# Optimization experiments

Hardware: AMD Instinct MI355X
Metric: run time of the kernel (lower is better)

Reference implementation:

```python
import jax, jax.numpy as jnp
import numpy as np

WS = 7          # window size
HEADS = 8
SHIFT = WS // 2  # shift=True -> 3
C = 256
KD = C // HEADS  # key_dim = 32
LN_EPS = 1e-3    # keras LayerNormalization default


def setup_inputs() -> dict:
    key = jax.random.key(0)
    ks = jax.random.split(key, 12)
    s = 1.0 / np.sqrt(C)
    x = jax.random.normal(ks[0], (16, 112, 112, C), dtype=jnp.float32)
    wq = jax.random.normal(ks[1], (C, HEADS, KD), dtype=jnp.float32) * s
    bq = jnp.zeros((HEADS, KD), dtype=jnp.float32)
    wk = jax.random.normal(ks[2], (C, HEADS, KD), dtype=jnp.float32) * s
    bk = jnp.zeros((HEADS, KD), dtype=jnp.float32)
    wv = jax.random.normal(ks[3], (C, HEADS, KD), dtype=jnp.float32) * s
    bv = jnp.zeros((HEADS, KD), dtype=jnp.float32)
    wo = jax.random.normal(ks[4], (HEADS, KD, C), dtype=jnp.float32) * s
    bo = jnp.zeros((C,), dtype=jnp.float32)
    gamma = jnp.ones((C,), dtype=jnp.float32)
    beta = jnp.zeros((C,), dtype=jnp.float32)
    return {"x": x, "wq": wq, "bq": bq, "wk": wk, "bk": bk,
            "wv": wv, "bv": bv, "wo": wo, "bo": bo,
            "gamma": gamma, "beta": beta}


def _swin_window_attn(x, wq, bq, wk, bk, wv, bv, wo, bo, gamma, beta):
    b, h, w, c = x.shape
    pad_h = (WS - h % WS) % WS
    pad_w = (WS - w % WS) % WS
    if pad_h or pad_w:
        x = jnp.pad(x, ((0, 0), (0, pad_h), (0, pad_w), (0, 0)))
    hp, wp = h + pad_h, w + pad_w
    if SHIFT > 0:
        x = jnp.roll(x, shift=(-SHIFT, -SHIFT), axis=(1, 2))
    nh, nw = hp // WS, wp // WS
    # window partition: (b, nh, WS, nw, WS, c) -> (b*nh*nw, WS*WS, c)
    win = x.reshape(b, nh, WS, nw, WS, c).transpose(0, 1, 3, 2, 4, 5)
    win = win.reshape(b * nh * nw, WS * WS, c)
    # multi-head attention (keras MHA: query scaled by 1/sqrt(key_dim))
    q = jnp.einsum("nsc,chd->nshd", win, wq) + bq
    k = jnp.einsum("nsc,chd->nshd", win, wk) + bk
    v = jnp.einsum("nsc,chd->nshd", win, wv) + bv
    scores = jnp.einsum("nqhd,nkhd->nhqk", q, k) / jnp.sqrt(jnp.float32(KD)).astype(q.dtype)
    probs = jax.nn.softmax(scores, axis=-1)
    ctx = jnp.einsum("nhqk,nkhd->nqhd", probs, v)
    attn = jnp.einsum("nqhd,hdc->nqc", ctx, wo) + bo
    # residual + LayerNorm
    y = attn + win
    mu = jnp.mean(y, axis=-1, keepdims=True)
    var = jnp.mean(jnp.square(y - mu), axis=-1, keepdims=True)
    y = (y - mu) * jax.lax.rsqrt(var + LN_EPS) * gamma + beta
    # window reverse
    out = y.reshape(b, nh, nw, WS, WS, c).transpose(0, 1, 3, 2, 4, 5)
    out = out.reshape(b, hp, wp, c)
    if SHIFT > 0:
        out = jnp.roll(out, shift=(SHIFT, SHIFT), axis=(1, 2))
    if pad_h or pad_w:
        out = out[:, :h, :w, :]
    return out


def reference(x, wq, bq, wk, bk, wv, bv, wo, bo, gamma, beta):
    return _swin_window_attn(x, wq, bq, wk, bk, wv, bv, wo, bo, gamma, beta)
```

## Files before the change

### kernel.cpp

```cpp
#include <hip/hip_runtime.h>
#include <hip/hip_bf16.h>

typedef __attribute__((ext_vector_type(8))) short short8;
typedef __attribute__((ext_vector_type(4))) short short4v;
typedef __attribute__((ext_vector_type(4))) float float4v;

#define LDS_BYTES 144384
#define XBF_OFF   0
#define VT_OFF    33792
#define Q_OFF     70656
#define K_OFF     104448
#define P_OFF     70656
#define CTX_OFF   33792
#define Y_OFF     70656

__device__ __forceinline__ unsigned short f2bf(float f) {
    union { float f; unsigned int u; } v; v.f = f;
    unsigned int r = v.u + 0x7FFFu + ((v.u >> 16) & 1u);
    return (unsigned short)(r >> 16);
}
__device__ __forceinline__ float bf2f(unsigned short h) {
    union { unsigned int u; float f; } v; v.u = ((unsigned int)h) << 16;
    return v.f;
}

__global__ void prep_weights(const float* __restrict__ wq, const float* __restrict__ wk,
                             const float* __restrict__ wv, const float* __restrict__ wo,
                             unsigned short* __restrict__ wfrag) {
    int tid = blockIdx.x * 256 + threadIdx.x;
    if (tid >= 4 * 65536) return;
    int m = tid >> 16;
    int e = tid & 65535;
    int j = e & 7;
    int lane = (e >> 3) & 63;
    int nt2 = (e >> 9) & 15;
    int ks = e >> 13;
    int c = ks * 32 + (lane >> 4) * 8 + j;
    int o = nt2 * 16 + (lane & 15);
    const float* W = (m == 0) ? wq : (m == 1) ? wk : (m == 2) ? wv : wo;
    wfrag[tid] = f2bf(W[c * 256 + o]);
}

__global__ __launch_bounds__(1024, 4) void swin_fused(
    const float* __restrict__ x,
    const unsigned short* __restrict__ wfrag,
    const float* __restrict__ bq, const float* __restrict__ bk,
    const float* __restrict__ bv, const float* __restrict__ bo,
    const float* __restrict__ gamma, const float* __restrict__ beta,
    float* __restrict__ out)
{
    extern __shared__ char smem[];
    const int tid = threadIdx.x;
    const int w    = tid >> 6;
    const int h    = w & 7;
    const int half = w >> 3;
    const int l   = tid & 63;
    const int l15 = l & 15;
    const int l4  = l >> 4;
    const int nt2 = 2 * h + half;

    const int blk = blockIdx.x;
    const int bb  = blk >> 8;
    const int wh  = (blk >> 4) & 15;
    const int ww  = blk & 15;

    unsigned short* Xbf = (unsigned short*)(smem + XBF_OFF);

    for (int idx = tid; idx < 64 * 64; idx += 1024) {
        const int tok = idx >> 6;
        const int c4  = idx & 63;
        float4v f = (float4v){0.f, 0.f, 0.f, 0.f};
        if (tok < 49) {
            const int i = tok / 7;
            const int j = tok - 7 * i;
            int gr = wh * 7 + i + 3; if (gr >= 112) gr -= 112;
            int gc = ww * 7 + j + 3; if (gc >= 112) gc -= 112;
            f = *(const float4v*)(x + (((size_t)bb * 112 + gr) * 112 + gc) * 256 + c4 * 4);
        }
        short4v hv;
        hv.x = (short)f2bf(f.x); hv.y = (short)f2bf(f.y);
        hv.z = (short)f2bf(f.z); hv.w = (short)f2bf(f.w);
        *(short4v*)(Xbf + tok * 264 + c4 * 4) = hv;
    }
    __syncthreads();

    unsigned short* Qs = (unsigned short*)(smem + Q_OFF);
    unsigned short* Ks = (unsigned short*)(smem + K_OFF);
    unsigned short* Vt = (unsigned short*)(smem + VT_OFF);

    const float* biases[3] = { bq, bk, bv };
#pragma unroll
    for (int m = 0; m < 3; ++m) {
        float4v acc[4];
#pragma unroll
        for (int mt = 0; mt < 4; ++mt) acc[mt] = (float4v){0.f, 0.f, 0.f, 0.f};
        const unsigned short* wmat = wfrag + m * 65536;
#pragma unroll
        for (int ks = 0; ks < 8; ++ks) {
            short8 bfr = *(const short8*)(wmat + ((ks * 16 + nt2) * 64 + l) * 8);
#pragma unroll
            for (int mt = 0; mt < 4; ++mt) {
                short8 afr = *(const short8*)(Xbf + (mt * 16 + l15) * 264 + ks * 32 + l4 * 8);
                acc[mt] = __builtin_amdgcn_mfma_f32_16x16x32_bf16(afr, bfr, acc[mt], 0, 0, 0);
            }
        }
        const int o = nt2 * 16 + l15;
        const float bias = biases[m][o];
        if (m == 2) {
            const int d = half * 16 + l15;
#pragma unroll
            for (int mt = 0; mt < 4; ++mt) {
                short4v hv;
                hv.x = (short)f2bf(acc[mt][0] + bias);
                hv.y = (short)f2bf(acc[mt][1] + bias);
                hv.z = (short)f2bf(acc[mt][2] + bias);
                hv.w = (short)f2bf(acc[mt][3] + bias);
                *(short4v*)(Vt + h * 2304 + d * 72 + mt * 16 + l4 * 4) = hv;
            }
        } else {
            unsigned short* dst = (m == 0) ? Qs : Ks;
#pragma unroll
            for (int mt = 0; mt < 4; ++mt) {
                const int tok0 = mt * 16 + l4 * 4;
                dst[(tok0 + 0) * 264 + o] = f2bf(acc[mt][0] + bias);
                dst[(tok0 + 1) * 264 + o] = f2bf(acc[mt][1] + bias);
                dst[(tok0 + 2) * 264 + o] = f2bf(acc[mt][2] + bias);
                dst[(tok0 + 3) * 264 + o] = f2bf(acc[mt][3] + bias);
            }
        }
    }
    __syncthreads();

    float4v sa[4][2];
#pragma unroll
    for (int mt = 0; mt < 4; ++mt)
#pragma unroll
        for (int nt = 0; nt < 2; ++nt)
            sa[mt][nt] = (float4v){0.f, 0.f, 0.f, 0.f};
    {
        short8 kfr[4], qfr[2];
#pragma unroll
        for (int mt = 0; mt < 4; ++mt)
            kfr[mt] = *(const short8*)(Ks + (mt * 16 + l15) * 264 + 32 * h + l4 * 8);
#pragma unroll
        for (int nt = 0; nt < 2; ++nt)
            qfr[nt] = *(const short8*)(Qs + (32 * half + nt * 16 + l15) * 264 + 32 * h + l4 * 8);
#pragma unroll
        for (int mt = 0; mt < 4; ++mt)
#pragma unroll
            for (int nt = 0; nt < 2; ++nt)
                sa[mt][nt] = __builtin_amdgcn_mfma_f32_16x16x32_bf16(kfr[mt], qfr[nt], sa[mt][nt], 0, 0, 0);
    }
    __syncthreads();

    unsigned short* Ph = (unsigned short*)(smem + P_OFF) + h * 4608;
    const float SCALE = 0.17677669529663687f;
#pragma unroll
    for (int nt = 0; nt < 2; ++nt) {
        float sv[4][4];
        float mx = -1e30f;
#pragma unroll
        for (int mt = 0; mt < 4; ++mt)
#pragma unroll
            for (int r = 0; r < 4; ++r) {
                const bool valid = (mt < 3) || ((l4 == 0) && (r == 0));
                sv[mt][r] = valid ? sa[mt][nt][r] * SCALE : -1e30f;
                mx = fmaxf(mx, sv[mt][r]);
            }
        mx = fmaxf(mx, __shfl_xor(mx, 16, 64));
        mx = fmaxf(mx, __shfl_xor(mx, 32, 64));
        float p[4][4];
        float sum = 0.f;
#pragma unroll
        for (int mt = 0; mt < 4; ++mt)
#pragma unroll
            for (int r = 0; r < 4; ++r) {
                p[mt][r] = __expf(sv[mt][r] - mx);
                sum += p[mt][r];
            }
        sum += __shfl_xor(sum, 16, 64);
        sum += __shfl_xor(sum, 32, 64);
        const float inv = 1.f / sum;
        const int q = 32 * half + nt * 16 + l15;
#pragma unroll
        for (int mt = 0; mt < 4; ++mt) {
            short4v hv;
            hv.x = (short)f2bf(p[mt][0] * inv);
            hv.y = (short)f2bf(p[mt][1] * inv);
            hv.z = (short)f2bf(p[mt][2] * inv);
            hv.w = (short)f2bf(p[mt][3] * inv);
            *(short4v*)(Ph + q * 72 + mt * 16 + l4 * 4) = hv;
        }
    }

    float4v ca[2][2];
#pragma unroll
    for (int mtl = 0; mtl < 2; ++mtl)
#pragma unroll
        for (int nt = 0; nt < 2; ++nt)
            ca[mtl][nt] = (float4v){0.f, 0.f, 0.f, 0.f};
#pragma unroll
    for (int ks = 0; ks < 2; ++ks) {
        short8 afr[2];
#pragma unroll
        for (int mtl = 0; mtl < 2; ++mtl)
            afr[mtl] = *(const short8*)(Ph + (32 * half + mtl * 16 + l15) * 72 + ks * 32 + l4 * 8);
#pragma unroll
        for (int nt = 0; nt < 2; ++nt) {
            short8 bfr = *(const short8*)(Vt + h * 2304 + (nt * 16 + l15) * 72 + ks * 32 + l4 * 8);
#pragma unroll
            for (int mtl = 0; mtl < 2; ++mtl)
                ca[mtl][nt] = __builtin_amdgcn_mfma_f32_16x16x32_bf16(afr[mtl], bfr, ca[mtl][nt], 0, 0, 0);
        }
    }
    __syncthreads();

    unsigned short* Ctx = (unsigned short*)(smem + CTX_OFF);
#pragma unroll
    for (int nt = 0; nt < 2; ++nt) {
        const int o = 32 * h + nt * 16 + l15;
#pragma unroll
        for (int mtl = 0; mtl < 2; ++mtl) {
            const int tok0 = (2 * half + mtl) * 16 + l4 * 4;
            Ctx[(tok0 + 0) * 264 + o] = f2bf(ca[mtl][nt][0]);
            Ctx[(tok0 + 1) * 264 + o] = f2bf(ca[mtl][nt][1]);
            Ctx[(tok0 + 2) * 264 + o] = f2bf(ca[mtl][nt][2]);
            Ctx[(tok0 + 3) * 264 + o] = f2bf(ca[mtl][nt][3]);
        }
    }
    __syncthreads();

    float4v oa[4];
#pragma unroll
    for (int mt = 0; mt < 4; ++mt) oa[mt] = (float4v){0.f, 0.f, 0.f, 0.f};
    const unsigned short* womat = wfrag + 3 * 65536;
#pragma unroll
    for (int ks = 0; ks < 8; ++ks) {
        short8 bfr = *(const short8*)(womat + ((ks * 16 + nt2) * 64 + l) * 8);
#pragma unroll
        for (int mt = 0; mt < 4; ++mt) {
            short8 afr = *(const short8*)(Ctx + (mt * 16 + l15) * 264 + ks * 32 + l4 * 8);
            oa[mt] = __builtin_amdgcn_mfma_f32_16x16x32_bf16(afr, bfr, oa[mt], 0, 0, 0);
        }
    }
    float* Y = (float*)(smem + Y_OFF);
    {
        const int cout = nt2 * 16 + l15;
        const float bias = bo[cout];
#pragma unroll
        for (int mt = 0; mt < 4; ++mt)
#pragma unroll
            for (int r = 0; r < 4; ++r) {
                const int tok = mt * 16 + l4 * 4 + r;
                const float xv = bf2f(Xbf[tok * 264 + cout]);
                Y[tok * 260 + cout] = oa[mt][r] + bias + xv;
            }
    }
    __syncthreads();

    const float4v g4  = *(const float4v*)(gamma + l * 4);
    const float4v be4 = *(const float4v*)(beta + l * 4);
#pragma unroll
    for (int t = 0; t < 4; ++t) {
        const int tok = w + t * 16;
        if (tok < 49) {
            float4v f = *(const float4v*)(Y + tok * 260 + l * 4);
            float sum = f.x + f.y + f.z + f.w;
            float sq  = f.x * f.x + f.y * f.y + f.z * f.z + f.w * f.w;
#pragma unroll
            for (int msk = 1; msk < 64; msk <<= 1) {
                sum += __shfl_xor(sum, msk, 64);
                sq  += __shfl_xor(sq,  msk, 64);
            }
            const float mu   = sum * (1.f / 256.f);
            const float var  = sq * (1.f / 256.f) - mu * mu;
            const float rstd = rsqrtf(var + 1e-3f);
            const int i = tok / 7;
            const int j = tok - 7 * i;
            int gr = wh * 7 + i + 3; if (gr >= 112) gr -= 112;
            int gc = ww * 7 + j + 3; if (gc >= 112) gc -= 112;
            float4v o4;
            o4.x = (f.x - mu) * rstd * g4.x + be4.x;
            o4.y = (f.y - mu) * rstd * g4.y + be4.y;
            o4.z = (f.z - mu) * rstd * g4.z + be4.z;
            o4.w = (f.w - mu) * rstd * g4.w + be4.w;
            *(float4v*)(out + (((size_t)bb * 112 + gr) * 112 + gc) * 256 + l * 4) = o4;
        }
    }
}

extern "C" void kernel_launch(void* const* d_in, const int* in_sizes, int n_in,
                              void* d_out, int out_size, void* d_ws, size_t ws_size,
                              hipStream_t stream) {
    const float* x     = (const float*)d_in[0];
    const float* wq    = (const float*)d_in[1];
    const float* bq    = (const float*)d_in[2];
    const float* wk    = (const float*)d_in[3];
    const float* bk    = (const float*)d_in[4];
    const float* wv    = (const float*)d_in[5];
    const float* bv    = (const float*)d_in[6];
    const float* wo    = (const float*)d_in[7];
    const float* bo    = (const float*)d_in[8];
    const float* gamma = (const float*)d_in[9];
    const float* beta  = (const float*)d_in[10];
    float* out = (float*)d_out;
    unsigned short* wfrag = (unsigned short*)d_ws;

    prep_weights<<<1024, 256, 0, stream>>>(wq, wk, wv, wo, wfrag);

    hipFuncSetAttribute((const void*)swin_fused,
                        hipFuncAttributeMaxDynamicSharedMemorySize, LDS_BYTES);
    swin_fused<<<4096, 1024, LDS_BYTES, stream>>>(x, wfrag, bq, bk, bv, bo, gamma, beta, out);
}
```

Measured before the change: 302.8 us.

## XOR-swizzle LDS row layout, use packed bf16 conversions, raise MFMA wave priority

```diff
diff --git a/kernel.cpp b/kernel.cpp
--- a/kernel.cpp
+++ b/kernel.cpp
@@ -4,6 +4,7 @@
 typedef __attribute__((ext_vector_type(8))) short short8;
 typedef __attribute__((ext_vector_type(4))) short short4v;
 typedef __attribute__((ext_vector_type(4))) float float4v;
+typedef __attribute__((ext_vector_type(2))) unsigned int uint2v;
 
 #define LDS_BYTES 144384
 #define XBF_OFF   0
@@ -14,10 +15,16 @@
 #define CTX_OFF   33792
 #define Y_OFF     70656
 
-__device__ __forceinline__ unsigned short f2bf(float f) {
-    union { float f; unsigned int u; } v; v.f = f;
-    unsigned int r = v.u + 0x7FFFu + ((v.u >> 16) & 1u);
-    return (unsigned short)(r >> 16);
+
+__device__ __forceinline__ unsigned short f2bf_rn(float f) {
+    union { __hip_bfloat16 b; unsigned short u; } v;
+    v.b = __float2bfloat16(f);
+    return v.u;
+}
+__device__ __forceinline__ unsigned int pk2bf(float a, float b) {
+    union { __hip_bfloat162 h; unsigned int u; } v;
+    v.h = __float22bfloat162_rn(make_float2(a, b));
+    return v.u;
 }
 __device__ __forceinline__ float bf2f(unsigned short h) {
     union { unsigned int u; float f; } v; v.u = ((unsigned int)h) << 16;
@@ -38,7 +45,7 @@
     int c = ks * 32 + (lane >> 4) * 8 + j;
     int o = nt2 * 16 + (lane & 15);
     const float* W = (m == 0) ? wq : (m == 1) ? wk : (m == 2) ? wv : wo;
-    wfrag[tid] = f2bf(W[c * 256 + o]);
+    wfrag[tid] = f2bf_rn(W[c * 256 + o]);
 }
 
 __global__ __launch_bounds__(1024, 4) void swin_fused(
@@ -59,12 +66,15 @@
     const int l4  = l >> 4;
     const int nt2 = 2 * h + half;
 
+    const int sxA = (l15 & 8) << 2;
+    const int sxS = (l4  & 2) << 4;
+
     const int blk = blockIdx.x;
     const int bb  = blk >> 8;
     const int wh  = (blk >> 4) & 15;
     const int ww  = blk & 15;
 
-    unsigned short* Xbf = (unsigned short*)(smem + XBF_OFF);
+    char* XbfC = smem + XBF_OFF;
 
     for (int idx = tid; idx < 64 * 64; idx += 1024) {
         const int tok = idx >> 6;
@@ -77,15 +87,15 @@
             int gc = ww * 7 + j + 3; if (gc >= 112) gc -= 112;
             f = *(const float4v*)(x + (((size_t)bb * 112 + gr) * 112 + gc) * 256 + c4 * 4);
         }
-        short4v hv;
-        hv.x = (short)f2bf(f.x); hv.y = (short)f2bf(f.y);
-        hv.z = (short)f2bf(f.z); hv.w = (short)f2bf(f.w);
-        *(short4v*)(Xbf + tok * 264 + c4 * 4) = hv;
-    }
-    __syncthreads();
-
-    unsigned short* Qs = (unsigned short*)(smem + Q_OFF);
-    unsigned short* Ks = (unsigned short*)(smem + K_OFF);
+        uint2v u;
+        u.x = pk2bf(f.x, f.y);
+        u.y = pk2bf(f.z, f.w);
+        *(uint2v*)(XbfC + ((tok * 528 + c4 * 8) ^ ((tok & 8) << 2))) = u;
+    }
+    __syncthreads();
+
+    char* QsC = smem + Q_OFF;
+    char* KsC = smem + K_OFF;
     unsigned short* Vt = (unsigned short*)(smem + VT_OFF);
 
     const float* biases[3] = { bq, bk, bv };
@@ -95,37 +105,36 @@
 #pragma unroll
         for (int mt = 0; mt < 4; ++mt) acc[mt] = (float4v){0.f, 0.f, 0.f, 0.f};
         const unsigned short* wmat = wfrag + m * 65536;
+        __builtin_amdgcn_s_setprio(1);
 #pragma unroll
         for (int ks = 0; ks < 8; ++ks) {
             short8 bfr = *(const short8*)(wmat + ((ks * 16 + nt2) * 64 + l) * 8);
 #pragma unroll
             for (int mt = 0; mt < 4; ++mt) {
-                short8 afr = *(const short8*)(Xbf + (mt * 16 + l15) * 264 + ks * 32 + l4 * 8);
+                short8 afr = *(const short8*)(XbfC + (((mt * 16 + l15) * 528 + (ks * 32 + l4 * 8) * 2) ^ sxA));
                 acc[mt] = __builtin_amdgcn_mfma_f32_16x16x32_bf16(afr, bfr, acc[mt], 0, 0, 0);
             }
         }
+        __builtin_amdgcn_s_setprio(0);
         const int o = nt2 * 16 + l15;
         const float bias = biases[m][o];
         if (m == 2) {
             const int d = half * 16 + l15;
 #pragma unroll
             for (int mt = 0; mt < 4; ++mt) {
-                short4v hv;
-                hv.x = (short)f2bf(acc[mt][0] + bias);
-                hv.y = (short)f2bf(acc[mt][1] + bias);
-                hv.z = (short)f2bf(acc[mt][2] + bias);
-                hv.w = (short)f2bf(acc[mt][3] + bias);
-                *(short4v*)(Vt + h * 2304 + d * 72 + mt * 16 + l4 * 4) = hv;
+                uint2v u;
+                u.x = pk2bf(acc[mt][0] + bias, acc[mt][1] + bias);
+                u.y = pk2bf(acc[mt][2] + bias, acc[mt][3] + bias);
+                *(uint2v*)(Vt + h * 2304 + d * 72 + mt * 16 + l4 * 4) = u;
             }
         } else {
-            unsigned short* dst = (m == 0) ? Qs : Ks;
+            char* dst = (m == 0) ? QsC : KsC;
 #pragma unroll
             for (int mt = 0; mt < 4; ++mt) {
                 const int tok0 = mt * 16 + l4 * 4;
-                dst[(tok0 + 0) * 264 + o] = f2bf(acc[mt][0] + bias);
-                dst[(tok0 + 1) * 264 + o] = f2bf(acc[mt][1] + bias);
-                dst[(tok0 + 2) * 264 + o] = f2bf(acc[mt][2] + bias);
-                dst[(tok0 + 3) * 264 + o] = f2bf(acc[mt][3] + bias);
+#pragma unroll
+                for (int r = 0; r < 4; ++r)
+                    *(unsigned short*)(dst + (((tok0 + r) * 528 + o * 2) ^ sxS)) = f2bf_rn(acc[mt][r] + bias);
             }
         }
     }
@@ -141,15 +150,17 @@
         short8 kfr[4], qfr[2];
 #pragma unroll
         for (int mt = 0; mt < 4; ++mt)
-            kfr[mt] = *(const short8*)(Ks + (mt * 16 + l15) * 264 + 32 * h + l4 * 8);
+            kfr[mt] = *(const short8*)(KsC + (((mt * 16 + l15) * 528 + (32 * h + l4 * 8) * 2) ^ sxA));
 #pragma unroll
         for (int nt = 0; nt < 2; ++nt)
-            qfr[nt] = *(const short8*)(Qs + (32 * half + nt * 16 + l15) * 264 + 32 * h + l4 * 8);
+            qfr[nt] = *(const short8*)(QsC + (((32 * half + nt * 16 + l15) * 528 + (32 * h + l4 * 8) * 2) ^ sxA));
+        __builtin_amdgcn_s_setprio(1);
 #pragma unroll
         for (int mt = 0; mt < 4; ++mt)
 #pragma unroll
             for (int nt = 0; nt < 2; ++nt)
                 sa[mt][nt] = __builtin_amdgcn_mfma_f32_16x16x32_bf16(kfr[mt], qfr[nt], sa[mt][nt], 0, 0, 0);
+        __builtin_amdgcn_s_setprio(0);
     }
     __syncthreads();
 
@@ -184,12 +195,10 @@
         const int q = 32 * half + nt * 16 + l15;
 #pragma unroll
         for (int mt = 0; mt < 4; ++mt) {
-            short4v hv;
-            hv.x = (short)f2bf(p[mt][0] * inv);
-            hv.y = (short)f2bf(p[mt][1] * inv);
-            hv.z = (short)f2bf(p[mt][2] * inv);
-            hv.w = (short)f2bf(p[mt][3] * inv);
-            *(short4v*)(Ph + q * 72 + mt * 16 + l4 * 4) = hv;
+            uint2v u;
+            u.x = pk2bf(p[mt][0] * inv, p[mt][1] * inv);
+            u.y = pk2bf(p[mt][2] * inv, p[mt][3] * inv);
+            *(uint2v*)(Ph + q * 72 + mt * 16 + l4 * 4) = u;
         }
     }
 
@@ -205,6 +214,7 @@
 #pragma unroll
         for (int mtl = 0; mtl < 2; ++mtl)
             afr[mtl] = *(const short8*)(Ph + (32 * half + mtl * 16 + l15) * 72 + ks * 32 + l4 * 8);
+        __builtin_amdgcn_s_setprio(1);
 #pragma unroll
         for (int nt = 0; nt < 2; ++nt) {
             short8 bfr = *(const short8*)(Vt + h * 2304 + (nt * 16 + l15) * 72 + ks * 32 + l4 * 8);
@@ -212,20 +222,20 @@
             for (int mtl = 0; mtl < 2; ++mtl)
                 ca[mtl][nt] = __builtin_amdgcn_mfma_f32_16x16x32_bf16(afr[mtl], bfr, ca[mtl][nt], 0, 0, 0);
         }
-    }
-    __syncthreads();
-
-    unsigned short* Ctx = (unsigned short*)(smem + CTX_OFF);
+        __builtin_amdgcn_s_setprio(0);
+    }
+    __syncthreads();
+
+    char* CtxC = smem + CTX_OFF;
 #pragma unroll
     for (int nt = 0; nt < 2; ++nt) {
         const int o = 32 * h + nt * 16 + l15;
 #pragma unroll
         for (int mtl = 0; mtl < 2; ++mtl) {
             const int tok0 = (2 * half + mtl) * 16 + l4 * 4;
-            Ctx[(tok0 + 0) * 264 + o] = f2bf(ca[mtl][nt][0]);
-            Ctx[(tok0 + 1) * 264 + o] = f2bf(ca[mtl][nt][1]);
-            Ctx[(tok0 + 2) * 264 + o] = f2bf(ca[mtl][nt][2]);
-            Ctx[(tok0 + 3) * 264 + o] = f2bf(ca[mtl][nt][3]);
+#pragma unroll
+            for (int r = 0; r < 4; ++r)
+                *(unsigned short*)(CtxC + (((tok0 + r) * 528 + o * 2) ^ sxS)) = f2bf_rn(ca[mtl][nt][r]);
         }
     }
     __syncthreads();
@@ -234,15 +244,17 @@
 #pragma unroll
     for (int mt = 0; mt < 4; ++mt) oa[mt] = (float4v){0.f, 0.f, 0.f, 0.f};
     const unsigned short* womat = wfrag + 3 * 65536;
+    __builtin_amdgcn_s_setprio(1);
 #pragma unroll
     for (int ks = 0; ks < 8; ++ks) {
         short8 bfr = *(const short8*)(womat + ((ks * 16 + nt2) * 64 + l) * 8);
 #pragma unroll
         for (int mt = 0; mt < 4; ++mt) {
-            short8 afr = *(const short8*)(Ctx + (mt * 16 + l15) * 264 + ks * 32 + l4 * 8);
+            short8 afr = *(const short8*)(CtxC + (((mt * 16 + l15) * 528 + (ks * 32 + l4 * 8) * 2) ^ sxA));
             oa[mt] = __builtin_amdgcn_mfma_f32_16x16x32_bf16(afr, bfr, oa[mt], 0, 0, 0);
         }
     }
+    __builtin_amdgcn_s_setprio(0);
     float* Y = (float*)(smem + Y_OFF);
     {
         const int cout = nt2 * 16 + l15;
@@ -252,7 +264,7 @@
 #pragma unroll
             for (int r = 0; r < 4; ++r) {
                 const int tok = mt * 16 + l4 * 4 + r;
-                const float xv = bf2f(Xbf[tok * 264 + cout]);
+                const float xv = bf2f(*(const unsigned short*)(XbfC + ((tok * 528 + cout * 2) ^ sxS)));
                 Y[tok * 260 + cout] = oa[mt][r] + bias + xv;
             }
     }
```

Result: no change. 301.0 us (-0.6%).
